# Performance work log

Measured on AMD Instinct MI355X. Metric: run time of the kernel, lower is better.

## Reference

```python
import jax, jax.numpy as jnp
import numpy as np

H = 150  # hidden_size


def setup_inputs() -> dict:
    key = jax.random.key(0)
    ks = jax.random.split(key, 6)
    B, T, D = 64, 2048, 150
    xs = jax.random.normal(ks[0], (B, T, D), jnp.float32)
    # Concatenated LSTM gate weights in order [i, f, g, o] (matches flax
    # LSTMCell's four separate Dense layers; input denses have no bias,
    # hidden denses carry the bias, zero-initialized by default).
    Wx0 = jax.random.normal(ks[1], (D, 4 * H), jnp.float32) / np.sqrt(D)
    Wh0 = jax.random.normal(ks[2], (H, 4 * H), jnp.float32) / np.sqrt(H)
    b0 = jnp.zeros((4 * H,), jnp.float32)
    Wx1 = jax.random.normal(ks[3], (H, 4 * H), jnp.float32) / np.sqrt(H)
    Wh1 = jax.random.normal(ks[4], (H, 4 * H), jnp.float32) / np.sqrt(H)
    b1 = jnp.zeros((4 * H,), jnp.float32)
    return dict(xs=xs, Wx0=Wx0, Wh0=Wh0, b0=b0, Wx1=Wx1, Wh1=Wh1, b1=b1)


def _lstm_layer(xs, Wx, Wh, b):
    # xs: [B, T, D]. Precompute the input projection as one big GEMM; the
    # recurrence only carries the small [B, H] @ [H, 4H] hidden GEMM.
    B = xs.shape[0]
    Hh = Wh.shape[0]
    x_proj = jnp.einsum('btd,dk->btk', xs, Wx)  # [B, T, 4H]

    def step(carry, xp):
        c, h = carry
        z = xp + h @ Wh + b  # [B, 4H]
        i, f, g, o = jnp.split(z, 4, axis=-1)
        i = jax.nn.sigmoid(i)
        f = jax.nn.sigmoid(f)
        g = jnp.tanh(g)
        o = jax.nn.sigmoid(o)
        new_c = f * c + i * g
        new_h = o * jnp.tanh(new_c)
        return (new_c, new_h), new_h

    c0 = jnp.zeros((B, Hh), xs.dtype)
    h0 = jnp.zeros((B, Hh), xs.dtype)
    _, ys = jax.lax.scan(step, (c0, h0), jnp.swapaxes(x_proj, 0, 1))  # [T, B, H]
    return jnp.swapaxes(ys, 0, 1)  # [B, T, H]


def reference(xs, Wx0, Wh0, b0, Wx1, Wh1, b1):
    ys = _lstm_layer(xs, Wx0, Wh0, b0)   # layer 0 (lstm_net)
    ys = _lstm_layer(ys, Wx1, Wh1, b1)   # additional layer
    return ys
```

## Files before the change

### kernel.cpp

```cpp
#include <hip/hip_runtime.h>
#include <cmath>

#define HID 150
#define FOURH 600
#define BATCH 64
#define TLEN 2048
#define NKS 5

typedef _Float16 f16;
typedef __attribute__((ext_vector_type(2))) _Float16 half2_t;
typedef __attribute__((ext_vector_type(8))) _Float16 f16x8;
typedef __attribute__((ext_vector_type(4))) float f32x4;

#if defined(__has_builtin)
#if __has_builtin(__builtin_amdgcn_fdot2)
#define FDOT2(a, b, c) __builtin_amdgcn_fdot2((a), (b), (c), false)
#endif
#endif
#ifndef FDOT2
__device__ __forceinline__ float fdot2_fb(half2_t a, half2_t b, float c) {
    return c + (float)a.x * (float)b.x + (float)a.y * (float)b.y;
}
#define FDOT2(a, b, c) fdot2_fb((a), (b), (c))
#endif

__device__ __forceinline__ float sigmoidf_(float x) {
    return 1.0f / (1.0f + __expf(-x));
}
__device__ __forceinline__ float tanhf_(float x) {
    return 1.0f - 2.0f / (__expf(2.0f * x) + 1.0f);
}


__global__ void pack_wh(const float* __restrict__ Wh0, const float* __restrict__ Wh1,
                        half2_t* __restrict__ whp) {
    int idx = blockIdx.x * 256 + threadIdx.x;
    if (idx >= 2 * 48000) return;
    int layer = idx / 48000, r = idx - layer * 48000;
    int j = r % HID, t = r / HID;
    int p = t & 15, gks = t >> 4;
    int g = gks & 3, ks = gks >> 2;
    const float* Wh = layer ? Wh1 : Wh0;
    int k0 = ks * 32 + 2 * p;
    float a  = (k0 < HID)     ? Wh[(size_t)k0 * FOURH + g * HID + j]       : 0.f;
    float bb = (k0 + 1 < HID) ? Wh[(size_t)(k0 + 1) * FOURH + g * HID + j] : 0.f;
    half2_t h; h.x = (_Float16)a; h.y = (_Float16)bb;
    whp[idx] = h;
}

#define WXP_PER_LAYER (38 * 5 * 64 * 8)
__global__ void pack_wxm(const float* __restrict__ Wx0, const float* __restrict__ Wx1,
                         f16* __restrict__ dst) {
    int idx = blockIdx.x * 256 + threadIdx.x;
    if (idx >= 2 * WXP_PER_LAYER) return;
    int layer = idx / WXP_PER_LAYER, r = idx - layer * WXP_PER_LAYER;
    int e = r & 7;
    int lane = (r >> 3) & 63;
    int f = r >> 9;
    int k5 = f % 5, ct = f / 5;
    int n = ct * 16 + (lane & 15);
    int k = k5 * 32 + (lane >> 4) * 8 + e;
    const float* Wx = layer ? Wx1 : Wx0;
    float v = (n < FOURH && k < HID) ? Wx[(size_t)k * FOURH + n] : 0.f;
    dst[idx] = (f16)v;
}

__global__ __launch_bounds__(256) void xproj_mfma(
    int nA, const float* __restrict__ XA, const f16* __restrict__ wxA,
    const float* __restrict__ biasA, float* __restrict__ xdA, int tA,
    const float* __restrict__ XB, const f16* __restrict__ wxB,
    const float* __restrict__ biasB, float* __restrict__ xdB, int tB,
    int C)
{
    const int xg = C / 32;
    const int per = 64 * xg;
    int x = blockIdx.x;
    const int isB = (x >= nA * per) ? 1 : 0;
    if (isB) x -= nA * per;
    const float* X    = isB ? XB    : XA;
    const f16*   wx   = isB ? wxB   : wxA;
    const float* bias = isB ? biasB : biasA;
    float*       xd   = isB ? xdB   : xdA;
    const int    t0   = isB ? tB    : tA;

    const int b  = x / xg;
    const int i0 = (x - b * xg) * 32;
    const int tid = threadIdx.x;
    const int wv = tid >> 6;
    const int l  = tid & 63;

    __shared__ __align__(16) f16 Xs[32][168];

    const float* Xbase = X + ((size_t)(b * TLEN + t0 + i0)) * HID;
    #pragma unroll
    for (int it = 0; it < 20; ++it) {
        int idx = tid + it * 256;
        int r = idx / 160, k = idx - r * 160;
        Xs[r][k] = (f16)((k < HID) ? Xbase[(size_t)r * HID + k] : 0.f);
    }
    __syncthreads();

    f16x8 af[2][NKS];
    #pragma unroll
    for (int mt = 0; mt < 2; ++mt)
        #pragma unroll
        for (int k5 = 0; k5 < NKS; ++k5)
            af[mt][k5] = *(const f16x8*)&Xs[mt * 16 + (l & 15)][k5 * 32 + (l >> 4) * 8];

    const int n_lo = l & 15;
    const int r0 = (l >> 4) * 4;
    for (int ct = wv; ct < 38; ct += 4) {
        const f16* wb = wx + ((size_t)(ct * 5) * 64 + l) * 8;
        f32x4 acc0 = {0.f, 0.f, 0.f, 0.f};
        f32x4 acc1 = {0.f, 0.f, 0.f, 0.f};
        #pragma unroll
        for (int k5 = 0; k5 < NKS; ++k5) {
            f16x8 bf = *(const f16x8*)(wb + (size_t)k5 * 64 * 8);
            acc0 = __builtin_amdgcn_mfma_f32_16x16x32_f16(af[0][k5], bf, acc0, 0, 0, 0);
            acc1 = __builtin_amdgcn_mfma_f32_16x16x32_f16(af[1][k5], bf, acc1, 0, 0, 0);
        }
        const int n = ct * 16 + n_lo;
        if (n < FOURH) {
            float bv = bias[n];
            float* o = xd + ((size_t)b * C + i0) * FOURH + n;
            #pragma unroll
            for (int r = 0; r < 4; ++r) {
                o[(size_t)(r0 + r) * FOURH]      = acc0[r] + bv;
                o[(size_t)(16 + r0 + r) * FOURH] = acc1[r] + bv;
            }
        }
    }
}

#define WL(arr, G, P) arr[(P)] = Wj[((G) * 16 + (P)) * HID];
#define WL16(arr, G) WL(arr,G,0) WL(arr,G,1) WL(arr,G,2) WL(arr,G,3) WL(arr,G,4) \
  WL(arr,G,5) WL(arr,G,6) WL(arr,G,7) WL(arr,G,8) WL(arr,G,9) WL(arr,G,10) \
  WL(arr,G,11) WL(arr,G,12) WL(arr,G,13) WL(arr,G,14) WL(arr,G,15)

#define KEEP2(x) do { float _kf = __builtin_bit_cast(float, (x)); \
    asm("" : "+v"(_kf)); (x) = __builtin_bit_cast(half2_t, _kf); } while (0)
#define KEEP4(arr, B) KEEP2(arr[(B)+0]); KEEP2(arr[(B)+1]); KEEP2(arr[(B)+2]); KEEP2(arr[(B)+3]);
#define KEEP16(arr) KEEP4(arr,0) KEEP4(arr,4) KEEP4(arr,8) KEEP4(arr,12)

#define DOTQ(Q) { \
  float4 hv = *(const float4*)(const void*)&h16[ks * 32 + (Q) * 8]; \
  half2_t h0 = __builtin_bit_cast(half2_t, hv.x); \
  half2_t h1 = __builtin_bit_cast(half2_t, hv.y); \
  half2_t h2 = __builtin_bit_cast(half2_t, hv.z); \
  half2_t h3 = __builtin_bit_cast(half2_t, hv.w); \
  a0 = FDOT2(h0, w0[(Q)*4+0], a0); a0 = FDOT2(h1, w0[(Q)*4+1], a0); \
  a0 = FDOT2(h2, w0[(Q)*4+2], a0); a0 = FDOT2(h3, w0[(Q)*4+3], a0); \
  a1 = FDOT2(h0, w1[(Q)*4+0], a1); a1 = FDOT2(h1, w1[(Q)*4+1], a1); \
  a1 = FDOT2(h2, w1[(Q)*4+2], a1); a1 = FDOT2(h3, w1[(Q)*4+3], a1); \
  a2 = FDOT2(h0, w2[(Q)*4+0], a2); a2 = FDOT2(h1, w2[(Q)*4+1], a2); \
  a2 = FDOT2(h2, w2[(Q)*4+2], a2); a2 = FDOT2(h3, w2[(Q)*4+3], a2); \
  a3 = FDOT2(h0, w3[(Q)*4+0], a3); a3 = FDOT2(h1, w3[(Q)*4+1], a3); \
  a3 = FDOT2(h2, w3[(Q)*4+2], a3); a3 = FDOT2(h3, w3[(Q)*4+3], a3); }

__global__ __launch_bounds__(768)
__attribute__((amdgpu_waves_per_eu(3, 3)))
void lstm_recur2(const float* __restrict__ xpA, const half2_t* __restrict__ whpA,
                 float* __restrict__ stA, int t0A,
                 const float* __restrict__ xpB, const half2_t* __restrict__ whpB,
                 float* __restrict__ stB, int t0B,
                 float* __restrict__ out, int C)
{
    const int part = blockIdx.x >> 6;
    const int b = blockIdx.x & 63;
    const int tid = threadIdx.x;
    const int tidc = (tid < 750) ? tid : 749;
    const int ks = tidc / HID;
    const int j  = tidc - ks * HID;

    const float*   xp    = part ? xpB  : xpA;
    const half2_t* whp   = part ? whpB : whpA;
    float*         state = part ? stB  : stA;
    const int      t0    = part ? t0B  : t0A;

    __shared__ __align__(16) _Float16 h16[160];
    __shared__ __align__(16) float part_s[NKS][4][152];

    half2_t w0[16], w1[16], w2[16], w3[16];
    {
        const half2_t* Wj = whp + (size_t)ks * 9600 + j;
        WL16(w0, 0) WL16(w1, 1) WL16(w2, 2) WL16(w3, 3)
    }
    KEEP16(w0) KEEP16(w1) KEEP16(w2) KEEP16(w3)

    float cst = 0.f;
    if (tid < 160) {
        float hv = 0.f;
        if (t0 != 0 && tid < HID) {
            cst = state[b * 300 + tid];
            hv  = state[b * 300 + HID + tid];
        }
        h16[tid] = (_Float16)hv;
    }
    __syncthreads();

    const float* xpb = xp + (size_t)b * C * FOURH;
    float* outb = out + ((size_t)b * TLEN + t0) * HID;

    float xn0 = 0.f, xn1 = 0.f, xn2 = 0.f, xn3 = 0.f;
    if (tid < HID) {
        xn0 = xpb[tid];
        xn1 = xpb[HID + tid];
        xn2 = xpb[2 * HID + tid];
        xn3 = xpb[3 * HID + tid];
    }

    for (int i = 0; i < C; ++i) {
        if (tid < 750) {
            float a0 = 0.f, a1 = 0.f, a2 = 0.f, a3 = 0.f;
            DOTQ(0) DOTQ(1) DOTQ(2) DOTQ(3)
            part_s[ks][0][j] = a0;
            part_s[ks][1][j] = a1;
            part_s[ks][2][j] = a2;
            part_s[ks][3][j] = a3;
        }
        __syncthreads();

        if (tid < HID) {
            float p0 = xn0, p1 = xn1, p2 = xn2, p3 = xn3;
            if (i + 1 < C) {
                const float* p = &xpb[(size_t)(i + 1) * FOURH];
                xn0 = p[tid];
                xn1 = p[HID + tid];
                xn2 = p[2 * HID + tid];
                xn3 = p[3 * HID + tid];
            }
            float z0 = p0, z1 = p1, z2 = p2, z3 = p3;
            #pragma unroll
            for (int s = 0; s < NKS; ++s) {
                z0 += part_s[s][0][tid];
                z1 += part_s[s][1][tid];
                z2 += part_s[s][2][tid];
                z3 += part_s[s][3][tid];
            }
            float ig = sigmoidf_(z0);
            float fg = sigmoidf_(z1);
            float gg = tanhf_(z2);
            float og = sigmoidf_(z3);
            cst = fg * cst + ig * gg;
            float hn = og * tanhf_(cst);
            h16[tid] = (_Float16)hn;
            outb[(size_t)i * HID + tid] = hn;
        }
        __syncthreads();
    }

    if (tid < HID) {
        state[b * 300 + tid] = cst;
        state[b * 300 + HID + tid] = (float)h16[tid];
    }
}

extern "C" void kernel_launch(void* const* d_in, const int* in_sizes, int n_in,
                              void* d_out, int out_size, void* d_ws, size_t ws_size,
                              hipStream_t stream) {
    const float* xs  = (const float*)d_in[0];
    const float* Wx0 = (const float*)d_in[1];
    const float* Wh0 = (const float*)d_in[2];
    const float* b0  = (const float*)d_in[3];
    const float* Wx1 = (const float*)d_in[4];
    const float* Wh1 = (const float*)d_in[5];
    const float* b1  = (const float*)d_in[6];
    float* out = (float*)d_out;

    int C = 256;
    {
        size_t need = 2ull * BATCH * C * FOURH * 4 + 48000ull * 2 * 4
                    + 2ull * WXP_PER_LAYER * 2 + 2ull * BATCH * 300 * 4;
        if (need > ws_size) C = 128;
    }
    const size_t xpsz = (size_t)BATCH * C * FOURH * 4;
    char* p = (char*)d_ws;
    float* xp0 = (float*)p;      p += xpsz;
    float* xp1 = (float*)p;      p += xpsz;
    half2_t* whp = (half2_t*)p;  p += 96000ull * 4;
    f16* wxp = (f16*)p;          p += 2ull * WXP_PER_LAYER * 2;
    float* st0 = (float*)p;      p += (size_t)BATCH * 300 * 4;
    float* st1 = (float*)p;
    const half2_t* whp0 = whp;
    const half2_t* whp1 = whp + 48000;
    const f16* wxp0 = wxp;
    const f16* wxp1 = wxp + WXP_PER_LAYER;

    pack_wh<<<dim3((2 * 48000 + 255) / 256), dim3(256), 0, stream>>>(Wh0, Wh1, whp);
    pack_wxm<<<dim3((2 * WXP_PER_LAYER + 255) / 256), dim3(256), 0, stream>>>(Wx0, Wx1, wxp);

    const int nchunk = TLEN / C;
    const int xg = C / 32;

    for (int s = 0; s <= nchunk; ++s) {
        const int hasA = (s < nchunk) ? 1 : 0;
        const int hasB = (s >= 1) ? 1 : 0;
        xproj_mfma<<<dim3((hasA + hasB) * 64 * xg), dim3(256), 0, stream>>>(
            hasA, xs, wxp0, b0, xp0, s * C,
            out, wxp1, b1, xp1, (s - 1) * C, C);
        if (hasA && hasB)
            lstm_recur2<<<dim3(128), dim3(768), 0, stream>>>(
                xp0, whp0, st0, s * C, xp1, whp1, st1, (s - 1) * C, out, C);
        else if (hasA)
            lstm_recur2<<<dim3(64), dim3(768), 0, stream>>>(
                xp0, whp0, st0, s * C, xp0, whp0, st0, 0, out, C);
        else
            lstm_recur2<<<dim3(64), dim3(768), 0, stream>>>(
                xp1, whp1, st1, (s - 1) * C, xp1, whp1, st1, 0, out, C);
    }
}
```

Measured before the change: 2.265 ms.

## Process two batch rows per recurrent block, streaming Wh from global memory

Each recurrent block now handles two batch elements instead of one, halving the grid to 64 or 32 blocks. Wh weights are no longer held in registers; each step streams them as float4 loads from a repacked global layout, and each load is reused across both batch rows. This halves how often each weight is fetched and frees many registers, but it adds memory traffic on the serial critical path of every step and uses fewer CUs.

```diff
diff --git a/kernel.cpp b/kernel.cpp
--- a/kernel.cpp
+++ b/kernel.cpp
@@ -31,21 +31,24 @@
     return 1.0f - 2.0f / (__expf(2.0f * x) + 1.0f);
 }
 
-
-__global__ void pack_wh(const float* __restrict__ Wh0, const float* __restrict__ Wh1,
-                        half2_t* __restrict__ whp) {
+#define H2(x) __builtin_bit_cast(half2_t, (x))
+
+
+__global__ void pack_wh2(const float* __restrict__ Wh0, const float* __restrict__ Wh1,
+                         half2_t* __restrict__ dst) {
     int idx = blockIdx.x * 256 + threadIdx.x;
-    if (idx >= 2 * 48000) return;
+    if (idx >= 96000) return;
     int layer = idx / 48000, r = idx - layer * 48000;
-    int j = r % HID, t = r / HID;
-    int p = t & 15, gks = t >> 4;
-    int g = gks & 3, ks = gks >> 2;
+    int e = r & 3, f4 = r >> 2;
+    int f = f4 / 750, t = f4 - f * 750;
+    int ks = t / HID, j = t - ks * HID;
+    int Q = f >> 2, g = f & 3;
+    int k0 = ks * 32 + Q * 8 + 2 * e;
     const float* Wh = layer ? Wh1 : Wh0;
-    int k0 = ks * 32 + 2 * p;
     float a  = (k0 < HID)     ? Wh[(size_t)k0 * FOURH + g * HID + j]       : 0.f;
     float bb = (k0 + 1 < HID) ? Wh[(size_t)(k0 + 1) * FOURH + g * HID + j] : 0.f;
     half2_t h; h.x = (_Float16)a; h.y = (_Float16)bb;
-    whp[idx] = h;
+    dst[idx] = h;
 }
 
 #define WXP_PER_LAYER (38 * 5 * 64 * 8)
@@ -132,110 +135,110 @@
     }
 }
 
-#define WL(arr, G, P) arr[(P)] = Wj[((G) * 16 + (P)) * HID];
-#define WL16(arr, G) WL(arr,G,0) WL(arr,G,1) WL(arr,G,2) WL(arr,G,3) WL(arr,G,4) \
-  WL(arr,G,5) WL(arr,G,6) WL(arr,G,7) WL(arr,G,8) WL(arr,G,9) WL(arr,G,10) \
-  WL(arr,G,11) WL(arr,G,12) WL(arr,G,13) WL(arr,G,14) WL(arr,G,15)
-
-#define KEEP2(x) do { float _kf = __builtin_bit_cast(float, (x)); \
-    asm("" : "+v"(_kf)); (x) = __builtin_bit_cast(half2_t, _kf); } while (0)
-#define KEEP4(arr, B) KEEP2(arr[(B)+0]); KEEP2(arr[(B)+1]); KEEP2(arr[(B)+2]); KEEP2(arr[(B)+3]);
-#define KEEP16(arr) KEEP4(arr,0) KEEP4(arr,4) KEEP4(arr,8) KEEP4(arr,12)
-
-#define DOTQ(Q) { \
-  float4 hv = *(const float4*)(const void*)&h16[ks * 32 + (Q) * 8]; \
-  half2_t h0 = __builtin_bit_cast(half2_t, hv.x); \
-  half2_t h1 = __builtin_bit_cast(half2_t, hv.y); \
-  half2_t h2 = __builtin_bit_cast(half2_t, hv.z); \
-  half2_t h3 = __builtin_bit_cast(half2_t, hv.w); \
-  a0 = FDOT2(h0, w0[(Q)*4+0], a0); a0 = FDOT2(h1, w0[(Q)*4+1], a0); \
-  a0 = FDOT2(h2, w0[(Q)*4+2], a0); a0 = FDOT2(h3, w0[(Q)*4+3], a0); \
-  a1 = FDOT2(h0, w1[(Q)*4+0], a1); a1 = FDOT2(h1, w1[(Q)*4+1], a1); \
-  a1 = FDOT2(h2, w1[(Q)*4+2], a1); a1 = FDOT2(h3, w1[(Q)*4+3], a1); \
-  a2 = FDOT2(h0, w2[(Q)*4+0], a2); a2 = FDOT2(h1, w2[(Q)*4+1], a2); \
-  a2 = FDOT2(h2, w2[(Q)*4+2], a2); a2 = FDOT2(h3, w2[(Q)*4+3], a2); \
-  a3 = FDOT2(h0, w3[(Q)*4+0], a3); a3 = FDOT2(h1, w3[(Q)*4+1], a3); \
-  a3 = FDOT2(h2, w3[(Q)*4+2], a3); a3 = FDOT2(h3, w3[(Q)*4+3], a3); }
+#define D4(acc, hf, wf) \
+  acc = FDOT2(H2((hf).x), H2((wf).x), acc); \
+  acc = FDOT2(H2((hf).y), H2((wf).y), acc); \
+  acc = FDOT2(H2((hf).z), H2((wf).z), acc); \
+  acc = FDOT2(H2((hf).w), H2((wf).w), acc);
+
+#define PASS(gb) { \
+  float4 wa0 = Ws[(0 * 4 + (gb)) * 750 + tidc]; \
+  float4 wa1 = Ws[(1 * 4 + (gb)) * 750 + tidc]; \
+  float4 wa2 = Ws[(2 * 4 + (gb)) * 750 + tidc]; \
+  float4 wa3 = Ws[(3 * 4 + (gb)) * 750 + tidc]; \
+  float4 wb0 = Ws[(0 * 4 + (gb) + 1) * 750 + tidc]; \
+  float4 wb1 = Ws[(1 * 4 + (gb) + 1) * 750 + tidc]; \
+  float4 wb2 = Ws[(2 * 4 + (gb) + 1) * 750 + tidc]; \
+  float4 wb3 = Ws[(3 * 4 + (gb) + 1) * 750 + tidc]; \
+  float au = 0.f, av = 0.f, bu = 0.f, bv = 0.f; \
+  { float4 hu = *(const float4*)(const void*)&h16[0][ks * 32 + 0];  \
+    float4 hv = *(const float4*)(const void*)&h16[1][ks * 32 + 0];  \
+    D4(au, hu, wa0) D4(av, hv, wa0) D4(bu, hu, wb0) D4(bv, hv, wb0) } \
+  { float4 hu = *(const float4*)(const void*)&h16[0][ks * 32 + 8];  \
+    float4 hv = *(const float4*)(const void*)&h16[1][ks * 32 + 8];  \
+    D4(au, hu, wa1) D4(av, hv, wa1) D4(bu, hu, wb1) D4(bv, hv, wb1) } \
+  { float4 hu = *(const float4*)(const void*)&h16[0][ks * 32 + 16]; \
+    float4 hv = *(const float4*)(const void*)&h16[1][ks * 32 + 16]; \
+    D4(au, hu, wa2) D4(av, hv, wa2) D4(bu, hu, wb2) D4(bv, hv, wb2) } \
+  { float4 hu = *(const float4*)(const void*)&h16[0][ks * 32 + 24]; \
+    float4 hv = *(const float4*)(const void*)&h16[1][ks * 32 + 24]; \
+    D4(au, hu, wa3) D4(av, hv, wa3) D4(bu, hu, wb3) D4(bv, hv, wb3) } \
+  part_s[0][ks][(gb)][j]     = au; \
+  part_s[1][ks][(gb)][j]     = av; \
+  part_s[0][ks][(gb) + 1][j] = bu; \
+  part_s[1][ks][(gb) + 1][j] = bv; }
 
 __global__ __launch_bounds__(768)
 __attribute__((amdgpu_waves_per_eu(3, 3)))
-void lstm_recur2(const float* __restrict__ xpA, const half2_t* __restrict__ whpA,
+void lstm_recur4(const float* __restrict__ xpA, const float4* __restrict__ whsA,
                  float* __restrict__ stA, int t0A,
-                 const float* __restrict__ xpB, const half2_t* __restrict__ whpB,
+                 const float* __restrict__ xpB, const float4* __restrict__ whsB,
                  float* __restrict__ stB, int t0B,
                  float* __restrict__ out, int C)
 {
-    const int part = blockIdx.x >> 6;
-    const int b = blockIdx.x & 63;
+    const int part = blockIdx.x >> 5;
+    const int b0 = (blockIdx.x & 31) * 2;
     const int tid = threadIdx.x;
     const int tidc = (tid < 750) ? tid : 749;
     const int ks = tidc / HID;
     const int j  = tidc - ks * HID;
 
-    const float*   xp    = part ? xpB  : xpA;
-    const half2_t* whp   = part ? whpB : whpA;
-    float*         state = part ? stB  : stA;
-    const int      t0    = part ? t0B  : t0A;
-
-    __shared__ __align__(16) _Float16 h16[160];
-    __shared__ __align__(16) float part_s[NKS][4][152];
-
-    half2_t w0[16], w1[16], w2[16], w3[16];
-    {
-        const half2_t* Wj = whp + (size_t)ks * 9600 + j;
-        WL16(w0, 0) WL16(w1, 1) WL16(w2, 2) WL16(w3, 3)
-    }
-    KEEP16(w0) KEEP16(w1) KEEP16(w2) KEEP16(w3)
-
+    const float*  xp    = part ? xpB  : xpA;
+    const float4* Ws    = part ? whsB : whsA;
+    float*        state = part ? stB  : stA;
+    const int     t0    = part ? t0B  : t0A;
+
+    __shared__ __align__(16) _Float16 h16[2][160];
+    __shared__ __align__(16) float part_s[2][NKS][4][152];
+
+    const int tidb = (tid < 300) ? tid : 299;
+    const int bb = tidb / HID;
+    const int jj = tidb - bb * HID;
+
+    if (tid < 320) {
+        int hb = tid / 160, hj = tid - hb * 160;
+        float hv = 0.f;
+        if (t0 != 0 && hj < HID) hv = state[(b0 + hb) * 300 + HID + hj];
+        h16[hb][hj] = (_Float16)hv;
+    }
     float cst = 0.f;
-    if (tid < 160) {
-        float hv = 0.f;
-        if (t0 != 0 && tid < HID) {
-            cst = state[b * 300 + tid];
-            hv  = state[b * 300 + HID + tid];
-        }
-        h16[tid] = (_Float16)hv;
-    }
+    if (t0 != 0 && tid < 300) cst = state[(b0 + bb) * 300 + jj];
     __syncthreads();
 
-    const float* xpb = xp + (size_t)b * C * FOURH;
-    float* outb = out + ((size_t)b * TLEN + t0) * HID;
+    const float* xpb = xp + (size_t)(b0 + bb) * C * FOURH;
+    float* outb = out + ((size_t)(b0 + bb) * TLEN + t0) * HID;
 
     float xn0 = 0.f, xn1 = 0.f, xn2 = 0.f, xn3 = 0.f;
-    if (tid < HID) {
-        xn0 = xpb[tid];
-        xn1 = xpb[HID + tid];
-        xn2 = xpb[2 * HID + tid];
-        xn3 = xpb[3 * HID + tid];
+    if (tid < 300) {
+        xn0 = xpb[jj];
+        xn1 = xpb[HID + jj];
+        xn2 = xpb[2 * HID + jj];
+        xn3 = xpb[3 * HID + jj];
     }
 
     for (int i = 0; i < C; ++i) {
         if (tid < 750) {
-            float a0 = 0.f, a1 = 0.f, a2 = 0.f, a3 = 0.f;
-            DOTQ(0) DOTQ(1) DOTQ(2) DOTQ(3)
-            part_s[ks][0][j] = a0;
-            part_s[ks][1][j] = a1;
-            part_s[ks][2][j] = a2;
-            part_s[ks][3][j] = a3;
+            PASS(0)
+            PASS(2)
         }
         __syncthreads();
 
-        if (tid < HID) {
+        if (tid < 300) {
             float p0 = xn0, p1 = xn1, p2 = xn2, p3 = xn3;
             if (i + 1 < C) {
                 const float* p = &xpb[(size_t)(i + 1) * FOURH];
-                xn0 = p[tid];
-                xn1 = p[HID + tid];
-                xn2 = p[2 * HID + tid];
-                xn3 = p[3 * HID + tid];
+                xn0 = p[jj];
+                xn1 = p[HID + jj];
+                xn2 = p[2 * HID + jj];
+                xn3 = p[3 * HID + jj];
             }
             float z0 = p0, z1 = p1, z2 = p2, z3 = p3;
             #pragma unroll
             for (int s = 0; s < NKS; ++s) {
-                z0 += part_s[s][0][tid];
-                z1 += part_s[s][1][tid];
-                z2 += part_s[s][2][tid];
-                z3 += part_s[s][3][tid];
+                z0 += part_s[bb][s][0][jj];
+                z1 += part_s[bb][s][1][jj];
+                z2 += part_s[bb][s][2][jj];
+                z3 += part_s[bb][s][3][jj];
             }
             float ig = sigmoidf_(z0);
             float fg = sigmoidf_(z1);
@@ -243,15 +246,15 @@
             float og = sigmoidf_(z3);
             cst = fg * cst + ig * gg;
             float hn = og * tanhf_(cst);
-            h16[tid] = (_Float16)hn;
-            outb[(size_t)i * HID + tid] = hn;
+            h16[bb][jj] = (_Float16)hn;
+            outb[(size_t)i * HID + jj] = hn;
         }
         __syncthreads();
     }
 
-    if (tid < HID) {
-        state[b * 300 + tid] = cst;
-        state[b * 300 + HID + tid] = (float)h16[tid];
+    if (tid < 300) {
+        state[(b0 + bb) * 300 + jj] = cst;
+        state[(b0 + bb) * 300 + HID + jj] = (float)h16[bb][jj];
     }
 }
 
@@ -269,7 +272,7 @@
 
     int C = 256;
     {
-        size_t need = 2ull * BATCH * C * FOURH * 4 + 48000ull * 2 * 4
+        size_t need = 2ull * BATCH * C * FOURH * 4 + 96000ull * 4
                     + 2ull * WXP_PER_LAYER * 2 + 2ull * BATCH * 300 * 4;
         if (need > ws_size) C = 128;
     }
@@ -281,12 +284,12 @@
     f16* wxp = (f16*)p;          p += 2ull * WXP_PER_LAYER * 2;
     float* st0 = (float*)p;      p += (size_t)BATCH * 300 * 4;
     float* st1 = (float*)p;
-    const half2_t* whp0 = whp;
-    const half2_t* whp1 = whp + 48000;
+    const float4* whs0 = (const float4*)whp;
+    const float4* whs1 = (const float4*)(whp + 48000);
     const f16* wxp0 = wxp;
     const f16* wxp1 = wxp + WXP_PER_LAYER;
 
-    pack_wh<<<dim3((2 * 48000 + 255) / 256), dim3(256), 0, stream>>>(Wh0, Wh1, whp);
+    pack_wh2<<<dim3((96000 + 255) / 256), dim3(256), 0, stream>>>(Wh0, Wh1, whp);
     pack_wxm<<<dim3((2 * WXP_PER_LAYER + 255) / 256), dim3(256), 0, stream>>>(Wx0, Wx1, wxp);
 
     const int nchunk = TLEN / C;
@@ -299,13 +302,13 @@
             hasA, xs, wxp0, b0, xp0, s * C,
             out, wxp1, b1, xp1, (s - 1) * C, C);
         if (hasA && hasB)
-            lstm_recur2<<<dim3(128), dim3(768), 0, stream>>>(
-                xp0, whp0, st0, s * C, xp1, whp1, st1, (s - 1) * C, out, C);
+            lstm_recur4<<<dim3(64), dim3(768), 0, stream>>>(
+                xp0, whs0, st0, s * C, xp1, whs1, st1, (s - 1) * C, out, C);
         else if (hasA)
-            lstm_recur2<<<dim3(64), dim3(768), 0, stream>>>(
-                xp0, whp0, st0, s * C, xp0, whp0, st0, 0, out, C);
+            lstm_recur4<<<dim3(32), dim3(768), 0, stream>>>(
+                xp0, whs0, st0, s * C, xp0, whs0, st0, 0, out, C);
         else
-            lstm_recur2<<<dim3(64), dim3(768), 0, stream>>>(
-                xp1, whp1, st1, (s - 1) * C, xp1, whp1, st1, 0, out, C);
-    }
-}
+            lstm_recur4<<<dim3(32), dim3(768), 0, stream>>>(
+                xp1, whs1, st1, (s - 1) * C, xp1, whs1, st1, 0, out, C);
+    }
+}
```

After: 5.355 ms. +136.4%, slower.

## Stream recurrent weights from LDS and global each step instead of registers

Applied to the files above, without the earlier changes.

The recurrent Wh weights are repacked into float4 groups and no longer held in 64 VGPRs per thread. Half of them (6000 float4, 96 KB) are staged into LDS once per block, and the other half are reloaded from global/L2 on every timestep. This frees register pressure, but adds per-step LDS and global load latency to the serial recurrence critical path. The 96 KB LDS allocation per block may also limit residency.

```diff
diff --git a/kernel.cpp b/kernel.cpp
--- a/kernel.cpp
+++ b/kernel.cpp
@@ -31,21 +31,24 @@
     return 1.0f - 2.0f / (__expf(2.0f * x) + 1.0f);
 }
 
-
-__global__ void pack_wh(const float* __restrict__ Wh0, const float* __restrict__ Wh1,
-                        half2_t* __restrict__ whp) {
+#define H2(x) __builtin_bit_cast(half2_t, (x))
+
+
+__global__ void pack_wh2(const float* __restrict__ Wh0, const float* __restrict__ Wh1,
+                         half2_t* __restrict__ dst) {
     int idx = blockIdx.x * 256 + threadIdx.x;
-    if (idx >= 2 * 48000) return;
+    if (idx >= 96000) return;
     int layer = idx / 48000, r = idx - layer * 48000;
-    int j = r % HID, t = r / HID;
-    int p = t & 15, gks = t >> 4;
-    int g = gks & 3, ks = gks >> 2;
+    int e = r & 3, f4 = r >> 2;
+    int f = f4 / 750, t = f4 - f * 750;
+    int ks = t / HID, j = t - ks * HID;
+    int Q = f >> 2, g = f & 3;
+    int k0 = ks * 32 + Q * 8 + 2 * e;
     const float* Wh = layer ? Wh1 : Wh0;
-    int k0 = ks * 32 + 2 * p;
     float a  = (k0 < HID)     ? Wh[(size_t)k0 * FOURH + g * HID + j]       : 0.f;
     float bb = (k0 + 1 < HID) ? Wh[(size_t)(k0 + 1) * FOURH + g * HID + j] : 0.f;
     half2_t h; h.x = (_Float16)a; h.y = (_Float16)bb;
-    whp[idx] = h;
+    dst[idx] = h;
 }
 
 #define WXP_PER_LAYER (38 * 5 * 64 * 8)
@@ -132,36 +135,20 @@
     }
 }
 
-#define WL(arr, G, P) arr[(P)] = Wj[((G) * 16 + (P)) * HID];
-#define WL16(arr, G) WL(arr,G,0) WL(arr,G,1) WL(arr,G,2) WL(arr,G,3) WL(arr,G,4) \
-  WL(arr,G,5) WL(arr,G,6) WL(arr,G,7) WL(arr,G,8) WL(arr,G,9) WL(arr,G,10) \
-  WL(arr,G,11) WL(arr,G,12) WL(arr,G,13) WL(arr,G,14) WL(arr,G,15)
-
-#define KEEP2(x) do { float _kf = __builtin_bit_cast(float, (x)); \
-    asm("" : "+v"(_kf)); (x) = __builtin_bit_cast(half2_t, _kf); } while (0)
-#define KEEP4(arr, B) KEEP2(arr[(B)+0]); KEEP2(arr[(B)+1]); KEEP2(arr[(B)+2]); KEEP2(arr[(B)+3]);
-#define KEEP16(arr) KEEP4(arr,0) KEEP4(arr,4) KEEP4(arr,8) KEEP4(arr,12)
-
-#define DOTQ(Q) { \
-  float4 hv = *(const float4*)(const void*)&h16[ks * 32 + (Q) * 8]; \
-  half2_t h0 = __builtin_bit_cast(half2_t, hv.x); \
-  half2_t h1 = __builtin_bit_cast(half2_t, hv.y); \
-  half2_t h2 = __builtin_bit_cast(half2_t, hv.z); \
-  half2_t h3 = __builtin_bit_cast(half2_t, hv.w); \
-  a0 = FDOT2(h0, w0[(Q)*4+0], a0); a0 = FDOT2(h1, w0[(Q)*4+1], a0); \
-  a0 = FDOT2(h2, w0[(Q)*4+2], a0); a0 = FDOT2(h3, w0[(Q)*4+3], a0); \
-  a1 = FDOT2(h0, w1[(Q)*4+0], a1); a1 = FDOT2(h1, w1[(Q)*4+1], a1); \
-  a1 = FDOT2(h2, w1[(Q)*4+2], a1); a1 = FDOT2(h3, w1[(Q)*4+3], a1); \
-  a2 = FDOT2(h0, w2[(Q)*4+0], a2); a2 = FDOT2(h1, w2[(Q)*4+1], a2); \
-  a2 = FDOT2(h2, w2[(Q)*4+2], a2); a2 = FDOT2(h3, w2[(Q)*4+3], a2); \
-  a3 = FDOT2(h0, w3[(Q)*4+0], a3); a3 = FDOT2(h1, w3[(Q)*4+1], a3); \
-  a3 = FDOT2(h2, w3[(Q)*4+2], a3); a3 = FDOT2(h3, w3[(Q)*4+3], a3); }
+#define D4(acc, hf, wf) \
+  acc = FDOT2(H2((hf).x), H2((wf).x), acc); \
+  acc = FDOT2(H2((hf).y), H2((wf).y), acc); \
+  acc = FDOT2(H2((hf).z), H2((wf).z), acc); \
+  acc = FDOT2(H2((hf).w), H2((wf).w), acc);
+
+#define DQ(hq, wg0, wg1, wg2, wg3) \
+  D4(a0, hq, wg0) D4(a1, hq, wg1) D4(a2, hq, wg2) D4(a3, hq, wg3)
 
 __global__ __launch_bounds__(768)
 __attribute__((amdgpu_waves_per_eu(3, 3)))
-void lstm_recur2(const float* __restrict__ xpA, const half2_t* __restrict__ whpA,
+void lstm_recur5(const float* __restrict__ xpA, const float4* __restrict__ whsA,
                  float* __restrict__ stA, int t0A,
-                 const float* __restrict__ xpB, const half2_t* __restrict__ whpB,
+                 const float* __restrict__ xpB, const float4* __restrict__ whsB,
                  float* __restrict__ stB, int t0B,
                  float* __restrict__ out, int C)
 {
@@ -172,20 +159,16 @@
     const int ks = tidc / HID;
     const int j  = tidc - ks * HID;
 
-    const float*   xp    = part ? xpB  : xpA;
-    const half2_t* whp   = part ? whpB : whpA;
-    float*         state = part ? stB  : stA;
-    const int      t0    = part ? t0B  : t0A;
-
+    const float*  xp    = part ? xpB  : xpA;
+    const float4* Ws    = part ? whsB : whsA;
+    float*        state = part ? stB  : stA;
+    const int     t0    = part ? t0B  : t0A;
+
+    __shared__ __align__(16) float4 ldsw[6000];
     __shared__ __align__(16) _Float16 h16[160];
     __shared__ __align__(16) float part_s[NKS][4][152];
 
-    half2_t w0[16], w1[16], w2[16], w3[16];
-    {
-        const half2_t* Wj = whp + (size_t)ks * 9600 + j;
-        WL16(w0, 0) WL16(w1, 1) WL16(w2, 2) WL16(w3, 3)
-    }
-    KEEP16(w0) KEEP16(w1) KEEP16(w2) KEEP16(w3)
+    for (int x = tid; x < 6000; x += 768) ldsw[x] = Ws[x];
 
     float cst = 0.f;
     if (tid < 160) {
@@ -211,8 +194,31 @@
 
     for (int i = 0; i < C; ++i) {
         if (tid < 750) {
+            float4 g0 = Ws[ 8 * 750 + tidc];
+            float4 g1 = Ws[ 9 * 750 + tidc];
+            float4 g2 = Ws[10 * 750 + tidc];
+            float4 g3 = Ws[11 * 750 + tidc];
+            float4 g4 = Ws[12 * 750 + tidc];
+            float4 g5 = Ws[13 * 750 + tidc];
+            float4 g6 = Ws[14 * 750 + tidc];
+            float4 g7 = Ws[15 * 750 + tidc];
+            float4 l0 = ldsw[0 * 750 + tidc];
+            float4 l1 = ldsw[1 * 750 + tidc];
+            float4 l2 = ldsw[2 * 750 + tidc];
+            float4 l3 = ldsw[3 * 750 + tidc];
+            float4 l4 = ldsw[4 * 750 + tidc];
+            float4 l5 = ldsw[5 * 750 + tidc];
+            float4 l6 = ldsw[6 * 750 + tidc];
+            float4 l7 = ldsw[7 * 750 + tidc];
+            float4 h0 = *(const float4*)(const void*)&h16[ks * 32 + 0];
+            float4 h1 = *(const float4*)(const void*)&h16[ks * 32 + 8];
+            float4 h2 = *(const float4*)(const void*)&h16[ks * 32 + 16];
+            float4 h3 = *(const float4*)(const void*)&h16[ks * 32 + 24];
             float a0 = 0.f, a1 = 0.f, a2 = 0.f, a3 = 0.f;
-            DOTQ(0) DOTQ(1) DOTQ(2) DOTQ(3)
+            DQ(h0, l0, l1, l2, l3)
+            DQ(h2, g0, g1, g2, g3)
+            DQ(h1, l4, l5, l6, l7)
+            DQ(h3, g4, g5, g6, g7)
             part_s[ks][0][j] = a0;
             part_s[ks][1][j] = a1;
             part_s[ks][2][j] = a2;
@@ -269,7 +275,7 @@
 
     int C = 256;
     {
-        size_t need = 2ull * BATCH * C * FOURH * 4 + 48000ull * 2 * 4
+        size_t need = 2ull * BATCH * C * FOURH * 4 + 96000ull * 4
                     + 2ull * WXP_PER_LAYER * 2 + 2ull * BATCH * 300 * 4;
         if (need > ws_size) C = 128;
     }
@@ -281,12 +287,12 @@
     f16* wxp = (f16*)p;          p += 2ull * WXP_PER_LAYER * 2;
     float* st0 = (float*)p;      p += (size_t)BATCH * 300 * 4;
     float* st1 = (float*)p;
-    const half2_t* whp0 = whp;
-    const half2_t* whp1 = whp + 48000;
+    const float4* whs0 = (const float4*)whp;
+    const float4* whs1 = (const float4*)(whp + 48000);
     const f16* wxp0 = wxp;
     const f16* wxp1 = wxp + WXP_PER_LAYER;
 
-    pack_wh<<<dim3((2 * 48000 + 255) / 256), dim3(256), 0, stream>>>(Wh0, Wh1, whp);
+    pack_wh2<<<dim3((96000 + 255) / 256), dim3(256), 0, stream>>>(Wh0, Wh1, whp);
     pack_wxm<<<dim3((2 * WXP_PER_LAYER + 255) / 256), dim3(256), 0, stream>>>(Wx0, Wx1, wxp);
 
     const int nchunk = TLEN / C;
@@ -299,13 +305,13 @@
             hasA, xs, wxp0, b0, xp0, s * C,
             out, wxp1, b1, xp1, (s - 1) * C, C);
         if (hasA && hasB)
-            lstm_recur2<<<dim3(128), dim3(768), 0, stream>>>(
-                xp0, whp0, st0, s * C, xp1, whp1, st1, (s - 1) * C, out, C);
+            lstm_recur5<<<dim3(128), dim3(768), 0, stream>>>(
+                xp0, whs0, st0, s * C, xp1, whs1, st1, (s - 1) * C, out, C);
         else if (hasA)
-            lstm_recur2<<<dim3(64), dim3(768), 0, stream>>>(
-                xp0, whp0, st0, s * C, xp0, whp0, st0, 0, out, C);
+            lstm_recur5<<<dim3(64), dim3(768), 0, stream>>>(
+                xp0, whs0, st0, s * C, xp0, whs0, st0, 0, out, C);
         else
-            lstm_recur2<<<dim3(64), dim3(768), 0, stream>>>(
-                xp1, whp1, st1, (s - 1) * C, xp1, whp1, st1, 0, out, C);
-    }
-}
+            lstm_recur5<<<dim3(64), dim3(768), 0, stream>>>(
+                xp1, whs1, st1, (s - 1) * C, xp1, whs1, st1, 0, out, C);
+    }
+}
```

After: 3.213 ms. 41.9% more time.
